# Kernel optimization log

Measured on AMD Instinct MI355X. Metric: run time of the kernel, lower is better.

The kernel has to match this reference:

```python
import jax, jax.numpy as jnp
import numpy as np

EPS = 1e-8
ALPHA = 0.05          # params.alpha
K_STEPS = 10          # params.K
MB, C, M, N = 2, 3, 256, 256
P, KS = 32, 7         # n_filters, kernel_size
FKS = 5               # degradation filter size


def _corr(x, w, groups):
    # cross-correlation, SAME zero padding (odd kernels)
    pad = w.shape[-1] // 2
    return jax.lax.conv_general_dilated(
        x, w, (1, 1), [(pad, pad), (pad, pad)],
        dimension_numbers=('NCHW', 'OIHW', 'NCHW'),
        feature_group_count=groups)


def conv_fil(x, fil):
    # depthwise blur: util.conv(x, fil)
    c = x.shape[1]
    w = jnp.broadcast_to(fil, (c, 1) + fil.shape)
    return _corr(x, w, c)


def convT_fil(x, fil):
    # adjoint of conv_fil = correlation with flipped kernel
    return conv_fil(x, fil[::-1, ::-1])


def conv_CSC(a, B):
    # out[b,c] = sum_p corr(a[b,p,c], B[p,c]);  a: (mb,P,C,M,N)
    mb, p, c, m, n = a.shape
    x = a.transpose(0, 2, 1, 3, 4).reshape(mb, c * p, m, n)
    w = B.transpose(1, 0, 2, 3)  # (C, P, k, k), grouped over C
    return _corr(x, w, c)


def convT_CSC(r, B):
    # adjoint: out[b,p,c] = corr(r[b,c], flip(B[p,c]))
    mb, c, m, n = r.shape
    p, k = B.shape[0], B.shape[-1]
    w = B[:, :, ::-1, ::-1].transpose(1, 0, 2, 3).reshape(c * p, 1, k, k)
    y = _corr(r, w, c)
    return y.reshape(mb, c, p, m, n).transpose(0, 2, 1, 3, 4)


def D(x):
    # circular forward differences -> (mb, 2, C, M, N)
    return jnp.stack([jnp.roll(x, -1, axis=-2) - x,
                      jnp.roll(x, -1, axis=-1) - x], axis=1)


def Dt(y):
    # adjoint of D
    y0, y1 = y[:, 0], y[:, 1]
    return (jnp.roll(y0, 1, axis=-2) - y0) + (jnp.roll(y1, 1, axis=-1) - y1)


def soft(x, t):
    return jnp.sign(x) * jnp.maximum(jnp.abs(x) - t, 0.0)


def prox_l12(y, t):
    # group soft-threshold over the 2 gradient components (axis=1)
    nrm = jnp.sqrt(jnp.sum(y * y, axis=1, keepdims=True))
    return y * jnp.maximum(1.0 - t / jnp.maximum(nrm, EPS), 0.0)


def proj_l2ball(v, z, radius):
    # per-sample projection onto {u : ||u - z||_2 <= radius}
    r = v - z
    nrm = jnp.sqrt(jnp.sum(r * r, axis=(1, 2, 3), keepdims=True))
    return z + r * jnp.minimum(1.0, radius / jnp.maximum(nrm, EPS))


def setup_inputs() -> dict:
    key = jax.random.key(0)
    k1, k2, k3 = jax.random.split(key, 3)
    z = jax.random.uniform(k1, (MB, C, M, N), dtype=jnp.float32)
    B = 0.01 * jax.random.normal(k2, (P, C, KS, KS), dtype=jnp.float32)
    a_init = 0.01 * jax.random.normal(k3, (MB, P, C, M, N), dtype=jnp.float32)
    # normalized Gaussian blur (degradation filter)
    g = np.exp(-((np.arange(FKS) - FKS // 2) ** 2) / (2.0 * 1.5 ** 2))
    fil = np.outer(g, g).astype(np.float32)
    fil = jnp.asarray(fil / fil.sum())
    # util.calc_max_singular_P(B[:,0]) via FFT spectral norm of stacked conv ops
    Bh = np.fft.fft2(np.asarray(B[:, 0]), s=(64, 64))
    op_norm = float(np.sqrt(np.max(np.sum(np.abs(Bh) ** 2, axis=0))))
    beta = 1.0 + 2.0 * op_norm + op_norm ** 2
    g1 = 2.0 / beta * 0.9
    g2 = 2.0 / beta * 0.9
    g3 = 1.0 / ((1.0 + 8.0) * 0.9) * (1.0 / g1 - beta / 2.0)
    ones = jnp.ones(K_STEPS, jnp.float32)
    return {'z': z, 'a_init': a_init, 'B': B, 'fil': fil,
            'lam1': 0.01 * ones, 'lam2': 0.01 * ones,
            'gam1': g1 * ones, 'gam2': g2 * ones, 'gam3': g3 * ones}


def reference(z, a_init, B, fil, lam1, lam2, gam1, gam2, gam3):
    mb, c, m, n = z.shape
    epsilon = ALPHA * jnp.sqrt(jnp.float32(c * m * n))
    x0 = convT_fil(z, fil)
    y1_0 = jnp.zeros((mb, 2, c, m, n), z.dtype)
    y2_0 = jnp.zeros_like(z)

    def step(carry, p):
        x_bef, a_bef, y1_bef, y2_bef = carry
        l1, l2, g1, g2, g3 = p
        Ba = conv_CSC(a_bef, B)
        x = x_bef - g1 * (x_bef - Ba + Dt(y1_bef) + convT_fil(y2_bef, fil))
        x_aft = jnp.clip(x, 0.0, 1.0)  # ProxBoxConstraint
        a_aft = soft(a_bef + g2 * convT_CSC(x_bef - Ba, B), g2 * l1)
        v = 2.0 * x_aft - x_bef
        y1 = y1_bef + g3 * D(v)
        y1_aft = y1 - g3 * prox_l12(y1 / (g3 + EPS), l2 / (g3 + EPS))
        y2 = y2_bef + g3 * conv_fil(v, fil)
        y2_aft = y2 - g3 * proj_l2ball(y2 / (g3 + EPS), z, epsilon)
        return (x_aft, a_aft, y1_aft, y2_aft), None

    steps = jnp.stack([lam1, lam2, gam1, gam2, gam3], axis=1)  # (K,5)
    (x_fin, _, _, _), _ = jax.lax.scan(step, (x0, a_init, y1_0, y2_0), steps)
    return x_fin
```

## Files before the change

### kernel.cpp

```cpp
#include <hip/hip_runtime.h>

#define MBn 2
#define Cn 3
#define Mn 256
#define Nn 256
#define Pn 32
#define IMG   65536
#define CIMG  196608
#define XSZ   393216
#define ASZ   12582912
#define EPSf  1e-8f
#define NSTEP 10

#define HW 38
#define HP 42
#define HSZ (HW * HW)
#define ASTR 42

#define NCONV 3072
#define NAUP  6144

__global__ __launch_bounds__(256) void k_x0(const float* __restrict__ z, const float* __restrict__ fil,
                                            float* __restrict__ x0, float* __restrict__ x0c) {
    int idx = blockIdx.x * 256 + threadIdx.x;
    if (idx >= XSZ) return;
    int j = idx & 255, i = (idx >> 8) & 255, cm = idx >> 16;
    const float* zc = z + cm * IMG;
    float acc = 0.f;
    #pragma unroll
    for (int u = 0; u < 5; ++u) {
        int ii = i + 2 - u;
        if ((unsigned)ii >= (unsigned)Mn) continue;
        #pragma unroll
        for (int v = 0; v < 5; ++v) {
            int jj = j + 2 - v;
            if ((unsigned)jj >= (unsigned)Nn) continue;
            acc += fil[u * 5 + v] * zc[ii * Nn + jj];
        }
    }
    x0[idx] = acc;
    x0c[idx] = acc;
}

__global__ __launch_bounds__(256, 4) void k_conv(const float* __restrict__ a_in, const float* __restrict__ Bg,
                                                 float* __restrict__ Bap,
                                                 const float* __restrict__ part, float* __restrict__ scale2) {
    __shared__ float buf[2][HW * HP];
    int blk = blockIdx.x;
    int tid = threadIdx.x;

    if (blk >= NCONV) {
        float* red = buf[0];
        int mbi = blk - NCONV;
        float s = 0.f;
        for (int l = tid; l < 768; l += 256) s += part[mbi * 768 + l];
        red[tid] = s;
        __syncthreads();
        #pragma unroll
        for (int k = 128; k > 0; k >>= 1) {
            if (tid < k) red[tid] += red[tid + k];
            __syncthreads();
        }
        if (tid == 0) {
            float nrm = sqrtf(red[0]);
            float radius = 0.05f * sqrtf((float)CIMG);
            scale2[mbi] = fminf(1.f, radius / fmaxf(nrm, EPSf));
        }
        return;
    }

    int pg   = blk & 7;
    int tile = (blk >> 3) & 63;
    int cm   = blk >> 9;
    int c = cm % Cn, mb = cm / Cn;
    int i0 = (tile >> 3) * 32, j0 = (tile & 7) * 32;
    int tx = tid & 15, ty = tid >> 4;

    int ldsoff[6]; int goff[6]; bool val[6]; bool wm[6];
    #pragma unroll
    for (int k = 0; k < 6; ++k) {
        int l = tid + 256 * k;
        int r = l / HW, cc = l - r * HW;
        int gi = i0 + r - 3, gj = j0 + cc - 3;
        wm[k]  = (l < HSZ);
        val[k] = wm[k] && ((unsigned)gi < (unsigned)Mn) && ((unsigned)gj < (unsigned)Nn);
        ldsoff[k] = r * HP + cc;
        goff[k]   = gi * Nn + gj;
    }

    const float* abase = a_in + ((size_t)(mb * Pn + pg * 4) * Cn + c) * IMG;
    float rv[6];
    #pragma unroll
    for (int k = 0; k < 6; ++k) rv[k] = val[k] ? abase[goff[k]] : 0.f;

    float acc00 = 0.f, acc01 = 0.f, acc10 = 0.f, acc11 = 0.f;

    #pragma unroll 1
    for (int pi = 0; pi < 4; ++pi) {
        float* bufc = buf[pi & 1];
        #pragma unroll
        for (int k = 0; k < 6; ++k) if (wm[k]) bufc[ldsoff[k]] = rv[k];
        if (pi < 3) {
            const float* apn = abase + (size_t)(pi + 1) * (Cn * IMG);
            #pragma unroll
            for (int k = 0; k < 6; ++k) rv[k] = val[k] ? apn[goff[k]] : 0.f;
        }
        __syncthreads();
        const float* bp = Bg + ((pg * 4 + pi) * Cn + c) * 49;
        float bv[49];
        #pragma unroll
        for (int k = 0; k < 49; ++k) bv[k] = bp[k];
        #pragma unroll
        for (int r = 0; r < 8; ++r) {
            float w[8];
            const float* rowp = bufc + (2 * ty + r) * HP + 2 * tx;
            #pragma unroll
            for (int k = 0; k < 4; ++k) {
                float2 t = *(const float2*)(rowp + 2 * k);
                w[2 * k] = t.x; w[2 * k + 1] = t.y;
            }
            if (r <= 6) {
                #pragma unroll
                for (int v = 0; v < 7; ++v) {
                    float b = bv[r * 7 + v];
                    acc00 += w[v]     * b;
                    acc01 += w[v + 1] * b;
                }
            }
            if (r >= 1) {
                #pragma unroll
                for (int v = 0; v < 7; ++v) {
                    float b = bv[(r - 1) * 7 + v];
                    acc10 += w[v]     * b;
                    acc11 += w[v + 1] * b;
                }
            }
        }
    }
    float* out = Bap + pg * XSZ + cm * IMG;
    int oi = i0 + 2 * ty, oj = j0 + 2 * tx;
    { float2 st; st.x = acc00; st.y = acc01; *(float2*)(out + oi * Nn + oj) = st; }
    { float2 st; st.x = acc10; st.y = acc11; *(float2*)(out + (oi + 1) * Nn + oj) = st; }
}

__global__ __launch_bounds__(256) void k_xup(const float* __restrict__ xb, const float* __restrict__ Bap,
                                             const float* __restrict__ y1, const float* __restrict__ y2T,
                                             const float* __restrict__ x0c, const float* __restrict__ fil,
                                             const float* __restrict__ gam1, const float* __restrict__ gam3,
                                             const float* __restrict__ scale2, int step,
                                             float* __restrict__ xa, float* __restrict__ rr,
                                             float* __restrict__ vv) {
    int idx = blockIdx.x * 256 + threadIdx.x;
    if (idx >= XSZ) return;
    float g1 = gam1[step];
    int j = idx & 255, i = (idx >> 8) & 255, cm = idx >> 16;
    int mb = cm / Cn, c = cm - mb * Cn;

    float A = 0.f, Bz = 0.f;
    if (step > 0) {
        float g3p = gam3[step - 1];
        float invp = 1.f / (g3p + EPSf);
        float sc = scale2[mb];
        A  = 1.f - g3p * invp * sc;
        Bz = -g3p * (1.f - sc);
    }

    const float* y10 = y1 + (mb * 2) * CIMG + c * IMG;
    const float* y11 = y10 + CIMG;
    int im1 = (i == 0) ? Mn - 1 : i - 1;
    int jm1 = (j == 0) ? Nn - 1 : j - 1;
    float dt = y10[im1 * Nn + j] - y10[i * Nn + j] + y11[i * Nn + jm1] - y11[i * Nn + j];

    const float* Tc = y2T + cm * IMG;
    float cf = 0.f;
    #pragma unroll
    for (int u = 0; u < 5; ++u) {
        int ii = i + 2 - u;
        if ((unsigned)ii >= (unsigned)Mn) continue;
        #pragma unroll
        for (int v = 0; v < 5; ++v) {
            int jj = j + 2 - v;
            if ((unsigned)jj >= (unsigned)Nn) continue;
            cf += fil[u * 5 + v] * Tc[ii * Nn + jj];
        }
    }
    cf = A * cf + Bz * x0c[idx];

    float bav = 0.f;
    #pragma unroll
    for (int k = 0; k < 8; ++k) bav += Bap[k * XSZ + idx];
    float xv = xb[idx];
    float xn = xv - g1 * (xv - bav + dt + cf);
    xn = fminf(fmaxf(xn, 0.f), 1.f);
    xa[idx] = xn;
    rr[idx] = xv - bav;
    vv[idx] = 2.f * xn - xv;
}

__global__ __launch_bounds__(256) void k_aup(const float* __restrict__ a_in, float* __restrict__ a_out,
                                             const float* __restrict__ rr, const float* __restrict__ Bg,
                                             float* __restrict__ y1, float* __restrict__ y2T,
                                             const float* __restrict__ vv, const float* __restrict__ fil,
                                             const float* __restrict__ z,
                                             const float* __restrict__ lam1, const float* __restrict__ lam2,
                                             const float* __restrict__ gam2, const float* __restrict__ gam3,
                                             const float* __restrict__ scale2, int step,
                                             float* __restrict__ partial) {
    __shared__ float rs[70 * ASTR];
    int blk = blockIdx.x;
    int tid = threadIdx.x;

    {
        int p    = blk & 31;
        int tile = (blk >> 5) & 31;
        int cm   = blk >> 10;
        int c = cm % Cn, mb = cm / Cn;
        int i0 = (tile >> 3) * 64, j0 = (tile & 7) * 32;
        int tx = tid & 15, ty = tid >> 4;

        int oi = i0 + 4 * ty, oj = j0 + 2 * tx;
        size_t off0 = ((size_t)(mb * Pn + p) * Cn + c) * IMG + (size_t)oi * Nn + oj;

        float2 cur[4];
        #pragma unroll
        for (int ri = 0; ri < 4; ++ri) cur[ri] = *(const float2*)(a_in + off0 + (size_t)ri * Nn);

        const float* rp = rr + cm * IMG;
        for (int l = tid; l < 70 * 38; l += 256) {
            int r = l / 38, cc = l - r * 38;
            int gi = i0 + r - 3, gj = j0 + cc - 3;
            float v = 0.f;
            if ((unsigned)gi < (unsigned)Mn && (unsigned)gj < (unsigned)Nn) v = rp[gi * Nn + gj];
            rs[r * ASTR + cc] = v;
        }
        __syncthreads();

        const float* bp = Bg + (p * Cn + c) * 49;
        float acc[8];
        #pragma unroll
        for (int k = 0; k < 8; ++k) acc[k] = 0.f;

        #pragma unroll
        for (int r = 0; r < 10; ++r) {
            float w[8];
            const float* rowp = rs + (4 * ty + r) * ASTR + 2 * tx;
            #pragma unroll
            for (int k = 0; k < 4; ++k) {
                float2 t = *(const float2*)(rowp + 2 * k);
                w[2 * k] = t.x; w[2 * k + 1] = t.y;
            }
            #pragma unroll
            for (int ri = 0; ri < 4; ++ri) {
                int u = r - ri;
                if (u >= 0 && u <= 6) {
                    #pragma unroll
                    for (int v = 0; v < 7; ++v) {
                        float b = bp[(6 - u) * 7 + (6 - v)];
                        acc[ri * 2]     += w[v]     * b;
                        acc[ri * 2 + 1] += w[v + 1] * b;
                    }
                }
            }
        }

        float g2 = gam2[step], thr = g2 * lam1[step];
        #pragma unroll
        for (int ri = 0; ri < 4; ++ri) {
            float2 s;
            s.x = cur[ri].x + g2 * acc[ri * 2];
            s.y = cur[ri].y + g2 * acc[ri * 2 + 1];
            s.x = copysignf(fmaxf(fabsf(s.x) - thr, 0.f), s.x);
            s.y = copysignf(fmaxf(fabsf(s.y) - thr, 0.f), s.y);
            *(float2*)(a_out + off0 + (size_t)ri * Nn) = s;
        }
    }

    if (blk >= XSZ / 256) return;
    __syncthreads();
    {
        float* red = rs;
        int idx = blk * 256 + tid;
        float g3 = gam3[step], l2v = lam2[step];
        int j = idx & 255, i = (idx >> 8) & 255, cm = idx >> 16;
        int mb = cm / Cn, c = cm - mb * Cn;
        const float* vc = vv + cm * IMG;

        float A = 0.f, Bz = 0.f;
        if (step > 0) {
            float g3p = gam3[step - 1];
            float invp = 1.f / (g3p + EPSf);
            float sc = scale2[mb];
            A  = 1.f - g3p * invp * sc;
            Bz = -g3p * (1.f - sc);
        }

        int ip1 = (i == Mn - 1) ? 0 : i + 1;
        int jp1 = (j == Nn - 1) ? 0 : j + 1;
        float vij = vc[i * Nn + j];
        float d0 = vc[ip1 * Nn + j] - vij;
        float d1 = vc[i * Nn + jp1] - vij;
        float* y10 = y1 + (mb * 2) * CIMG + c * IMG + i * Nn + j;
        float* y11 = y10 + CIMG;
        float t0 = *y10 + g3 * d0;
        float t1 = *y11 + g3 * d1;
        float inv = 1.f / (g3 + EPSf);
        float w0 = t0 * inv, w1 = t1 * inv;
        float nrm = sqrtf(w0 * w0 + w1 * w1);
        float fac = fmaxf(1.f - (l2v * inv) / fmaxf(nrm, EPSf), 0.f);
        *y10 = t0 - g3 * (w0 * fac);
        *y11 = t1 - g3 * (w1 * fac);

        float cf = 0.f;
        #pragma unroll
        for (int u = 0; u < 5; ++u) {
            int ii2 = i + u - 2;
            if ((unsigned)ii2 >= (unsigned)Mn) continue;
            #pragma unroll
            for (int v = 0; v < 5; ++v) {
                int jj2 = j + v - 2;
                if ((unsigned)jj2 >= (unsigned)Nn) continue;
                cf += fil[u * 5 + v] * vc[ii2 * Nn + jj2];
            }
        }
        float zv = z[idx];
        float t = A * y2T[idx] + Bz * zv + g3 * cf;
        y2T[idx] = t;
        float d = t * inv - zv;
        red[tid] = d * d;
        __syncthreads();
        #pragma unroll
        for (int s = 128; s > 0; s >>= 1) {
            if (tid < s) red[tid] += red[tid + s];
            __syncthreads();
        }
        if (tid == 0) partial[blk] = red[0];
    }
}

extern "C" void kernel_launch(void* const* d_in, const int* in_sizes, int n_in,
                              void* d_out, int out_size, void* d_ws, size_t ws_size,
                              hipStream_t stream) {
    const float* z      = (const float*)d_in[0];
    const float* a_init = (const float*)d_in[1];
    const float* B      = (const float*)d_in[2];
    const float* fil    = (const float*)d_in[3];
    const float* lam1   = (const float*)d_in[4];
    const float* lam2   = (const float*)d_in[5];
    const float* gam1   = (const float*)d_in[6];
    const float* gam2   = (const float*)d_in[7];
    const float* gam3   = (const float*)d_in[8];

    float* ws = (float*)d_ws;
    float* a      = ws;
    float* xA     = a + ASZ;
    float* xB     = xA + XSZ;
    float* x0c    = xB + XSZ;
    float* Bap    = x0c + XSZ;
    float* rr     = Bap + 8 * XSZ;
    float* vv     = rr + XSZ;
    float* y1     = vv + XSZ;
    float* y2T    = y1 + 2 * XSZ;
    float* part   = y2T + XSZ;
    float* scale2 = part + 1536;

    hipMemsetAsync(y1, 0, (size_t)2 * XSZ * sizeof(float), stream);
    hipMemsetAsync(part, 0, 1536 * sizeof(float), stream);
    k_x0<<<XSZ / 256, 256, 0, stream>>>(z, fil, xA, x0c);

    float* xin = xA;
    float* xout = xB;
    for (int s = 0; s < NSTEP; ++s) {
        const float* a_src = (s == 0) ? a_init : a;
        k_conv<<<NCONV + 2, 256, 0, stream>>>(a_src, B, Bap, part, scale2);
        k_xup<<<XSZ / 256, 256, 0, stream>>>(xin, Bap, y1, y2T, x0c, fil, gam1, gam3, scale2, s,
                                             xout, rr, vv);
        if (s < NSTEP - 1) {
            k_aup<<<NAUP, 256, 0, stream>>>(a_src, a, rr, B, y1, y2T, vv, fil, z,
                                            lam1, lam2, gam2, gam3, scale2, s, part);
        }
        float* t = xin; xin = xout; xout = t;
    }

    hipMemcpyAsync(d_out, xin, (size_t)XSZ * sizeof(float), hipMemcpyDeviceToDevice, stream);
}
```

Before: 781.7 us.

## Enlarge CSC conv tile to 64x32 with four output rows per thread

The forward CSC convolution kernel now processes 64x32 output tiles, halving the block count, and each thread computes a 4x2 output patch instead of 2x2. This lowers halo overhead per output and reuses each LDS row load across more accumulators. Filter weights are now read directly from global memory inside the loop instead of being preloaded into 49 registers, and LDS use per block roughly doubles, which may reduce occupancy.

```diff
diff --git a/kernel.cpp b/kernel.cpp
--- a/kernel.cpp
+++ b/kernel.cpp
@@ -12,12 +12,13 @@
 #define EPSf  1e-8f
 #define NSTEP 10
 
-#define HW 38
-#define HP 42
-#define HSZ (HW * HW)
+#define CHW 38
+#define CHR 70
+#define CHP 42
+#define CHSZ (CHR * CHW)
 #define ASTR 42
 
-#define NCONV 3072
+#define NCONV 1536
 #define NAUP  6144
 
 __global__ __launch_bounds__(256) void k_x0(const float* __restrict__ z, const float* __restrict__ fil,
@@ -45,7 +46,7 @@
 __global__ __launch_bounds__(256, 4) void k_conv(const float* __restrict__ a_in, const float* __restrict__ Bg,
                                                  float* __restrict__ Bap,
                                                  const float* __restrict__ part, float* __restrict__ scale2) {
-    __shared__ float buf[2][HW * HP];
+    __shared__ float buf[2][CHR * CHP];
     int blk = blockIdx.x;
     int tid = threadIdx.x;
 
@@ -70,77 +71,74 @@
     }
 
     int pg   = blk & 7;
-    int tile = (blk >> 3) & 63;
-    int cm   = blk >> 9;
+    int tile = (blk >> 3) & 31;
+    int cm   = blk >> 8;
     int c = cm % Cn, mb = cm / Cn;
-    int i0 = (tile >> 3) * 32, j0 = (tile & 7) * 32;
+    int i0 = (tile >> 3) * 64, j0 = (tile & 7) * 32;
     int tx = tid & 15, ty = tid >> 4;
 
-    int ldsoff[6]; int goff[6]; bool val[6]; bool wm[6];
-    #pragma unroll
-    for (int k = 0; k < 6; ++k) {
+    int ldsoff[11]; int goff[11]; bool val[11]; bool wm[11];
+    #pragma unroll
+    for (int k = 0; k < 11; ++k) {
         int l = tid + 256 * k;
-        int r = l / HW, cc = l - r * HW;
+        int r = l / CHW, cc = l - r * CHW;
         int gi = i0 + r - 3, gj = j0 + cc - 3;
-        wm[k]  = (l < HSZ);
+        wm[k]  = (l < CHSZ);
         val[k] = wm[k] && ((unsigned)gi < (unsigned)Mn) && ((unsigned)gj < (unsigned)Nn);
-        ldsoff[k] = r * HP + cc;
+        ldsoff[k] = r * CHP + cc;
         goff[k]   = gi * Nn + gj;
     }
 
     const float* abase = a_in + ((size_t)(mb * Pn + pg * 4) * Cn + c) * IMG;
-    float rv[6];
-    #pragma unroll
-    for (int k = 0; k < 6; ++k) rv[k] = val[k] ? abase[goff[k]] : 0.f;
-
-    float acc00 = 0.f, acc01 = 0.f, acc10 = 0.f, acc11 = 0.f;
+    float rv[11];
+    #pragma unroll
+    for (int k = 0; k < 11; ++k) rv[k] = val[k] ? abase[goff[k]] : 0.f;
+
+    float acc[8];
+    #pragma unroll
+    for (int k = 0; k < 8; ++k) acc[k] = 0.f;
 
     #pragma unroll 1
     for (int pi = 0; pi < 4; ++pi) {
         float* bufc = buf[pi & 1];
         #pragma unroll
-        for (int k = 0; k < 6; ++k) if (wm[k]) bufc[ldsoff[k]] = rv[k];
+        for (int k = 0; k < 11; ++k) if (wm[k]) bufc[ldsoff[k]] = rv[k];
         if (pi < 3) {
             const float* apn = abase + (size_t)(pi + 1) * (Cn * IMG);
             #pragma unroll
-            for (int k = 0; k < 6; ++k) rv[k] = val[k] ? apn[goff[k]] : 0.f;
+            for (int k = 0; k < 11; ++k) rv[k] = val[k] ? apn[goff[k]] : 0.f;
         }
         __syncthreads();
-        const float* bp = Bg + ((pg * 4 + pi) * Cn + c) * 49;
-        float bv[49];
-        #pragma unroll
-        for (int k = 0; k < 49; ++k) bv[k] = bp[k];
-        #pragma unroll
-        for (int r = 0; r < 8; ++r) {
+        const float* bq = Bg + ((pg * 4 + pi) * Cn + c) * 49;
+        #pragma unroll
+        for (int r = 0; r < 10; ++r) {
             float w[8];
-            const float* rowp = bufc + (2 * ty + r) * HP + 2 * tx;
+            const float* rowp = bufc + (4 * ty + r) * CHP + 2 * tx;
             #pragma unroll
             for (int k = 0; k < 4; ++k) {
                 float2 t = *(const float2*)(rowp + 2 * k);
                 w[2 * k] = t.x; w[2 * k + 1] = t.y;
             }
-            if (r <= 6) {
-                #pragma unroll
-                for (int v = 0; v < 7; ++v) {
-                    float b = bv[r * 7 + v];
-                    acc00 += w[v]     * b;
-                    acc01 += w[v + 1] * b;
+            #pragma unroll
+            for (int ri = 0; ri < 4; ++ri) {
+                int u = r - ri;
+                if (u >= 0 && u <= 6) {
+                    #pragma unroll
+                    for (int v = 0; v < 7; ++v) {
+                        float b = bq[u * 7 + v];
+                        acc[ri * 2]     += w[v]     * b;
+                        acc[ri * 2 + 1] += w[v + 1] * b;
+                    }
                 }
             }
-            if (r >= 1) {
-                #pragma unroll
-                for (int v = 0; v < 7; ++v) {
-                    float b = bv[(r - 1) * 7 + v];
-                    acc10 += w[v]     * b;
-                    acc11 += w[v + 1] * b;
-                }
-            }
         }
     }
     float* out = Bap + pg * XSZ + cm * IMG;
-    int oi = i0 + 2 * ty, oj = j0 + 2 * tx;
-    { float2 st; st.x = acc00; st.y = acc01; *(float2*)(out + oi * Nn + oj) = st; }
-    { float2 st; st.x = acc10; st.y = acc11; *(float2*)(out + (oi + 1) * Nn + oj) = st; }
+    #pragma unroll
+    for (int ri = 0; ri < 4; ++ri) {
+        float2 st; st.x = acc[ri * 2]; st.y = acc[ri * 2 + 1];
+        *(float2*)(out + (size_t)(i0 + 4 * ty + ri) * Nn + j0 + 2 * tx) = st;
+    }
 }
 
 __global__ __launch_bounds__(256) void k_xup(const float* __restrict__ xb, const float* __restrict__ Bap,
```

Measured after the change: 746.4 us. -4.5%, faster.
